# Performance work log

Hardware: AMD Instinct MI355X
Metric: run time of the kernel (lower is better)

## Reference

```python
import jax, jax.numpy as jnp
import numpy as np

NODE_TYPES = ["drug", "protein", "side_effect", "pathway"]
N = {"drug": 20000, "protein": 50000, "side_effect": 10000, "pathway": 3000}
# (src_type, dst_type) for: treats, targets, in_pathway, causes, rev_treats, rev_targets, rev_in_pathway
RELS = [("drug", "side_effect"), ("drug", "protein"), ("protein", "pathway"),
        ("protein", "side_effect"), ("side_effect", "drug"), ("protein", "drug"),
        ("pathway", "protein")]
E = [500000, 400000, 150000, 400000, 500000, 400000, 150000]
D_IN, H, O = 128, 256, 256
EPS = 1e-5


def setup_inputs() -> dict:
    key = jax.random.key(0)
    ks = iter(jax.random.split(key, 64))
    inp = {}
    for t in NODE_TYPES:
        inp["x_" + t] = jax.random.normal(next(ks), (N[t], D_IN), jnp.float32)
    for i, (st, dt) in enumerate(RELS):
        inp[f"src_{i}"] = jax.random.randint(next(ks), (E[i],), 0, N[st], jnp.int32)
        inp[f"dst_{i}"] = jax.random.randint(next(ks), (E[i],), 0, N[dt], jnp.int32)
    sc1 = float(1.0 / np.sqrt(D_IN))
    sc2 = float(1.0 / np.sqrt(H))
    inp["W1l"] = jax.random.uniform(next(ks), (7, D_IN, H), jnp.float32, -sc1, sc1)
    inp["W1r"] = jax.random.uniform(next(ks), (7, D_IN, H), jnp.float32, -sc1, sc1)
    inp["b1"] = jax.random.uniform(next(ks), (7, H), jnp.float32, -sc1, sc1)
    inp["W2l"] = jax.random.uniform(next(ks), (7, H, O), jnp.float32, -sc2, sc2)
    inp["W2r"] = jax.random.uniform(next(ks), (7, H, O), jnp.float32, -sc2, sc2)
    inp["b2"] = jax.random.uniform(next(ks), (7, O), jnp.float32, -sc2, sc2)
    inp["g1"] = jnp.ones((H,), jnp.float32)
    inp["beta1"] = jnp.zeros((H,), jnp.float32)
    inp["g2"] = jnp.ones((O,), jnp.float32)
    inp["beta2"] = jnp.zeros((O,), jnp.float32)
    return inp


def _sage_layer(xs, srcs, dsts, Wl, Wr, b):
    # Hetero SAGEConv: per relation, mean-aggregate src features at dst,
    # project, add root transform; sum over relations per dst type.
    out = {t: None for t in NODE_TYPES}
    for i, (st, dt) in enumerate(RELS):
        msg = xs[st][srcs[i]]                                             # [E_i, d] gather
        s = jax.ops.segment_sum(msg, dsts[i], num_segments=N[dt])         # scatter-add
        cnt = jax.ops.segment_sum(jnp.ones((msg.shape[0], 1), msg.dtype),
                                  dsts[i], num_segments=N[dt])
        mean = s / jnp.maximum(cnt, 1.0)                                  # SAGE default aggr='mean'
        rel = mean @ Wl[i] + b[i] + xs[dt] @ Wr[i]                        # lin_l(agg) + lin_r(x_dst)
        out[dt] = rel if out[dt] is None else out[dt] + rel               # HeteroConv aggr='sum'
    return out


def _bn_relu(v, g, beta):
    # training-mode BatchNorm1d (biased variance) + ReLU
    mu = v.mean(0)
    var = v.var(0)
    return jax.nn.relu((v - mu) * jax.lax.rsqrt(var + EPS) * g + beta)


def reference(x_drug, x_protein, x_side_effect, x_pathway,
              W1l, W1r, b1, W2l, W2r, b2, g1, beta1, g2, beta2,
              src_0, dst_0, src_1, dst_1, src_2, dst_2, src_3, dst_3,
              src_4, dst_4, src_5, dst_5, src_6, dst_6):
    xs = {"drug": x_drug, "protein": x_protein,
          "side_effect": x_side_effect, "pathway": x_pathway}
    srcs = [src_0, src_1, src_2, src_3, src_4, src_5, src_6]
    dsts = [dst_0, dst_1, dst_2, dst_3, dst_4, dst_5, dst_6]
    h = _sage_layer(xs, srcs, dsts, W1l, W1r, b1)
    h = {t: _bn_relu(v, g1, beta1) for t, v in h.items()}
    h = _sage_layer(h, srcs, dsts, W2l, W2r, b2)
    h = {t: _bn_relu(v, g2, beta2) for t, v in h.items()}
    return (h["drug"], h["protein"], h["side_effect"], h["pathway"])
```

## Files before the change

### kernel.cpp

```cpp
#include <hip/hip_runtime.h>

#define EPS_BN 1e-5f

typedef short bf16x8 __attribute__((ext_vector_type(8)));
typedef float f32x4 __attribute__((ext_vector_type(4)));

__device__ __forceinline__ unsigned short f2b(float f)
{
    union { float f; unsigned int u; } c; c.f = f;
    unsigned int u = c.u + 0x7FFFu + ((c.u >> 16) & 1u);
    return (unsigned short)(u >> 16);
}
__device__ __forceinline__ float blo(unsigned int u)
{
    union { unsigned int u; float f; } c; c.u = u << 16; return c.f;
}
__device__ __forceinline__ float bhi(unsigned int u)
{
    union { unsigned int u; float f; } c; c.u = u & 0xFFFF0000u; return c.f;
}

__device__ __forceinline__ void async_ld16(const unsigned short* g, unsigned short* l)
{
    __builtin_amdgcn_global_load_lds(
        (const __attribute__((address_space(1))) unsigned int*)g,
        (__attribute__((address_space(3))) unsigned int*)l, 16, 0, 0);
}

__device__ __forceinline__ int relof_e(int e) {
    return (e>=500000)+(e>=900000)+(e>=1050000)+(e>=1450000)+(e>=1950000)+(e>=2350000);
}
__device__ __forceinline__ int relof_n(int i) {
    return (i>=10000)+(i>=60000)+(i>=63000)+(i>=73000)+(i>=93000)+(i>=113000);
}
__device__ __forceinline__ int eoff_of(int r) {
    return r<1?0 : r<2?500000 : r<3?900000 : r<4?1050000 : r<5?1450000 : r<6?1950000 : 2350000;
}
__device__ __forceinline__ int coff_of(int r) {
    return r<1?0 : r<2?10000 : r<3?60000 : r<4?63000 : r<5?73000 : r<6?93000 : 113000;
}
__device__ __forceinline__ int typ_of(int row) { return (row>=20000)+(row>=70000)+(row>=80000); }
__device__ __forceinline__ int nbound(int t)   { return t<1?20000 : t<2?70000 : t<3?80000 : 83000; }
__device__ __forceinline__ float invR_of(int t){ return t<1?5e-5f : t<2?2e-5f : t<3?1e-4f : (1.0f/3000.0f); }

struct Graph { const int* src[7]; const int* dst[7]; };

__device__ __forceinline__ void relptrs(const Graph& g, int r, const int*& sp, const int*& dp)
{
    sp = g.src[0]; dp = g.dst[0];
    if (r==1){sp=g.src[1];dp=g.dst[1];}
    if (r==2){sp=g.src[2];dp=g.dst[2];}
    if (r==3){sp=g.src[3];dp=g.dst[3];}
    if (r==4){sp=g.src[4];dp=g.dst[4];}
    if (r==5){sp=g.src[5];dp=g.dst[5];}
    if (r==6){sp=g.src[6];dp=g.dst[6];}
}

__global__ void count_all(Graph g, int* __restrict__ icnt)
{
    for (int e = blockIdx.x * blockDim.x + threadIdx.x; e < 2500000; e += gridDim.x * blockDim.x) {
        int r = relof_e(e);
        const int *sp, *dp; relptrs(g, r, sp, dp);
        int le = e - eoff_of(r);
        atomicAdd(&icnt[coff_of(r) + dp[le]], 1);
    }
}

__global__ __launch_bounds__(1024)
void scan1(const int* __restrict__ icnt, int* __restrict__ scanbuf, int* __restrict__ bsums)
{
    __shared__ int lds[1024];
    int tid = threadIdx.x;
    int gid = blockIdx.x * 1024 + tid;
    int v = (gid < 163000) ? icnt[gid] : 0;
    lds[tid] = v;
    __syncthreads();
    for (int d = 1; d < 1024; d <<= 1) {
        int t = (tid >= d) ? lds[tid - d] : 0;
        __syncthreads();
        lds[tid] += t;
        __syncthreads();
    }
    scanbuf[gid] = lds[tid];
    if (tid == 1023) bsums[blockIdx.x] = lds[1023];
}

__global__ __launch_bounds__(256)
void scan2(int* __restrict__ bsums)
{
    __shared__ int lds[256];
    int tid = threadIdx.x;
    int v = (tid < 160) ? bsums[tid] : 0;
    lds[tid] = v;
    __syncthreads();
    for (int d = 1; d < 256; d <<= 1) {
        int t = (tid >= d) ? lds[tid - d] : 0;
        __syncthreads();
        lds[tid] += t;
        __syncthreads();
    }
    bsums[tid] = tid ? lds[tid - 1] : 0;
}

__global__ __launch_bounds__(256)
void scan_fix(const int* __restrict__ icnt, const int* __restrict__ scanbuf,
              const int* __restrict__ bsums, int* __restrict__ rowptrG,
              int* __restrict__ cur, float* __restrict__ inv,
              unsigned char* __restrict__ sliceid)
{
    int idx = blockIdx.x * blockDim.x + threadIdx.x;
    if (idx > 163000) return;
    int G = bsums[idx >> 10] + ((idx & 1023) ? scanbuf[idx - 1] : 0);
    rowptrG[idx] = G;
    if (idx < 163000) {
        cur[idx] = G;
        inv[idx] = 1.0f / (float)max(icnt[idx], 1);
        int s = G / 312500;
        sliceid[idx] = (unsigned char)(s > 7 ? 7 : s);
    }
}

__global__ void fill_all(Graph g, const unsigned char* __restrict__ sliceid,
                         int* __restrict__ cur, int* __restrict__ csr)
{
    const int slice = blockIdx.x & 7;
    const int bper  = gridDim.x >> 3;
    const int bidx  = blockIdx.x >> 3;
    for (int e = bidx * blockDim.x + threadIdx.x; e < 2500000; e += bper * blockDim.x) {
        int r = relof_e(e);
        const int *sp, *dp; relptrs(g, r, sp, dp);
        int le = e - eoff_of(r);
        int gidx = coff_of(r) + dp[le];
        if (sliceid[gidx] == slice)
            csr[atomicAdd(&cur[gidx], 1)] = sp[le];
    }
}

__global__ void tob16_kernel(const float* __restrict__ in, unsigned short* __restrict__ out, int n4)
{
    for (int i = blockIdx.x * blockDim.x + threadIdx.x; i < n4; i += gridDim.x * blockDim.x) {
        float4 v = ((const float4*)in)[i];
        uint2 o;
        o.x = (unsigned int)f2b(v.x) | ((unsigned int)f2b(v.y) << 16);
        o.y = (unsigned int)f2b(v.z) | ((unsigned int)f2b(v.w) << 16);
        ((uint2*)out)[i] = o;
    }
}

struct GatherCfg {
    const unsigned short* X[7];
    const int* rowptrG;
    const int* csr;
    const float* inv;
    unsigned short* agg;
};

template <int D>
__global__ __launch_bounds__(256)
void gather_all(GatherCfg c)
{
    constexpr int LPE = D / 8;
    constexpr int EPW = 64 / LPE;
    int wid = (blockIdx.x * blockDim.x + threadIdx.x) >> 6;
    if (wid >= 163000) return;
    int l = threadIdx.x & 63;
    int q = l & (LPE - 1);
    int gg = l / LPE;
    int r = relof_n(wid);
    const unsigned short* X = c.X[0];
    if (r==1) X=c.X[1];
    if (r==2) X=c.X[2];
    if (r==3) X=c.X[3];
    if (r==4) X=c.X[4];
    if (r==5) X=c.X[5];
    if (r==6) X=c.X[6];
    const unsigned short* Xq = X + q * 8;
    const int* csr = c.csr;
    int beg = c.rowptrG[wid], end = c.rowptrG[wid + 1];
    float acc[8] = {0.f,0.f,0.f,0.f,0.f,0.f,0.f,0.f};
    int it = beg;
    for (; it + 4 * EPW <= end; it += 4 * EPW) {
        int s0 = csr[it + gg];
        int s1 = csr[it + EPW + gg];
        int s2 = csr[it + 2 * EPW + gg];
        int s3 = csr[it + 3 * EPW + gg];
        uint4 v0 = *(const uint4*)(Xq + (size_t)s0 * D);
        uint4 v1 = *(const uint4*)(Xq + (size_t)s1 * D);
        uint4 v2 = *(const uint4*)(Xq + (size_t)s2 * D);
        uint4 v3 = *(const uint4*)(Xq + (size_t)s3 * D);
        acc[0]+=blo(v0.x); acc[1]+=bhi(v0.x); acc[2]+=blo(v0.y); acc[3]+=bhi(v0.y);
        acc[4]+=blo(v0.z); acc[5]+=bhi(v0.z); acc[6]+=blo(v0.w); acc[7]+=bhi(v0.w);
        acc[0]+=blo(v1.x); acc[1]+=bhi(v1.x); acc[2]+=blo(v1.y); acc[3]+=bhi(v1.y);
        acc[4]+=blo(v1.z); acc[5]+=bhi(v1.z); acc[6]+=blo(v1.w); acc[7]+=bhi(v1.w);
        acc[0]+=blo(v2.x); acc[1]+=bhi(v2.x); acc[2]+=blo(v2.y); acc[3]+=bhi(v2.y);
        acc[4]+=blo(v2.z); acc[5]+=bhi(v2.z); acc[6]+=blo(v2.w); acc[7]+=bhi(v2.w);
        acc[0]+=blo(v3.x); acc[1]+=bhi(v3.x); acc[2]+=blo(v3.y); acc[3]+=bhi(v3.y);
        acc[4]+=blo(v3.z); acc[5]+=bhi(v3.z); acc[6]+=blo(v3.w); acc[7]+=bhi(v3.w);
    }
    for (; it < end; it += EPW) {
        int i0 = it + gg;
        if (i0 < end) {
            int s0 = csr[i0];
            uint4 v0 = *(const uint4*)(Xq + (size_t)s0 * D);
            acc[0]+=blo(v0.x); acc[1]+=bhi(v0.x); acc[2]+=blo(v0.y); acc[3]+=bhi(v0.y);
            acc[4]+=blo(v0.z); acc[5]+=bhi(v0.z); acc[6]+=blo(v0.w); acc[7]+=bhi(v0.w);
        }
    }
#pragma unroll
    for (int k = 0; k < 8; ++k) {
        if (LPE == 16) acc[k] += __shfl_xor(acc[k], 16);
        acc[k] += __shfl_xor(acc[k], 32);
    }
    if (l < LPE) {
        float inv = c.inv[wid];
        uint4 o;
        o.x = (unsigned int)f2b(acc[0]*inv) | ((unsigned int)f2b(acc[1]*inv) << 16);
        o.y = (unsigned int)f2b(acc[2]*inv) | ((unsigned int)f2b(acc[3]*inv) << 16);
        o.z = (unsigned int)f2b(acc[4]*inv) | ((unsigned int)f2b(acc[5]*inv) << 16);
        o.w = (unsigned int)f2b(acc[6]*inv) | ((unsigned int)f2b(acc[7]*inv) << 16);
        *(uint4*)(c.agg + (size_t)wid * D + q * 8) = o;
    }
}

__global__ void wtrans_kernel(const float* __restrict__ Wr, const float* __restrict__ Wl,
                              unsigned short* __restrict__ wsumT, unsigned short* __restrict__ WlT,
                              int K)
{
    const int nrel[4]  = {2, 2, 2, 1};
    const int rl[4][2] = {{4,5},{1,6},{0,3},{2,2}};
    int per = 256 * K;
    int tot = 11 * per;
    for (int idx = blockIdx.x * blockDim.x + threadIdx.x; idx < tot;
         idx += gridDim.x * blockDim.x) {
        if (idx < 4 * per) {
            int t = idx / per, rem = idx - t * per;
            int n = rem / K, k = rem - n * K;
            float s = Wr[(size_t)rl[t][0] * per + k * 256 + n];
            if (nrel[t] > 1) s += Wr[(size_t)rl[t][1] * per + k * 256 + n];
            wsumT[idx] = f2b(s);
        } else {
            int j = idx - 4 * per;
            int r = j / per, rem = j - r * per;
            int n = rem / K, k = rem - n * K;
            WlT[j] = f2b(Wl[(size_t)r * per + k * 256 + n]);
        }
    }
}

struct GemmBatch {
    const unsigned short* A0[4];
    const unsigned short* A1[4];
    const unsigned short* A2[4];
    const unsigned short* B0[4];
    const unsigned short* B1[4];
    const unsigned short* B2[4];
    float* outF;
    unsigned short* outB;
    int R[4]; int bcum[4]; int rowoff[4]; int nsrc[4];
    int K, kshift, outf32;
};

__global__ __launch_bounds__(512, 4)
void gemm_mfma(GemmBatch g)
{
    __shared__ __align__(16) unsigned short Atile[2][128 * 32];
    __shared__ __align__(16) unsigned short Btile[2][256 * 32];

    const int tid = threadIdx.x;
    const int bz = blockIdx.x;
    const int t = (bz >= g.bcum[1]) + (bz >= g.bcum[2]) + (bz >= g.bcum[3]);
    const int bm = (bz - g.bcum[t]) << 7;
    const int w = tid >> 6, l = tid & 63;
    const int wr = w >> 2, wc = w & 3;

    const int R = g.R[t];
    const int K = g.K, kshift = g.kshift, kmask = K - 1;
    const unsigned short* A0t = g.A0[t];
    const unsigned short* A1t = g.A1[t];
    const unsigned short* A2t = g.A2[t];
    const unsigned short* B0t = g.B0[t];
    const unsigned short* B1t = g.B1[t];
    const unsigned short* B2t = g.B2[t];
    const int steps = (g.nsrc[t] * K) >> 5;

    const int rloc = tid >> 2;
    const int swz  = (((tid & 3) ^ ((tid >> 3) & 3)) << 3);
    const int srowA = min(bm + rloc, R - 1);
    const int wseg  = w << 9;

    auto stage = [&](int st, int buf) {
        int kglob = st << 5;
        int s  = kglob >> kshift;
        int kk = kglob & kmask;
        const unsigned short* As = (s == 0) ? A0t : (s == 1) ? A1t : A2t;
        const unsigned short* Bs = (s == 0) ? B0t : (s == 1) ? B1t : B2t;
        async_ld16(As + (size_t)srowA * K + kk + swz, &Atile[buf][wseg]);
        async_ld16(Bs + (size_t)rloc  * K + kk + swz, &Btile[buf][wseg]);
        async_ld16(Bs + (size_t)(128 + rloc) * K + kk + swz, &Btile[buf][4096 + wseg]);
    };

    f32x4 acc[4][4];
#pragma unroll
    for (int i = 0; i < 4; ++i)
#pragma unroll
        for (int j = 0; j < 4; ++j)
            acc[i][j] = (f32x4){0.f, 0.f, 0.f, 0.f};

    const int ck = l >> 4;
    const int ra = wr * 64 + (l & 15);
    const int aoff = ra * 32 + ((ck ^ ((ra >> 1) & 3)) << 3);
    const int rb = wc * 64 + (l & 15);
    const int boff = rb * 32 + ((ck ^ ((rb >> 1) & 3)) << 3);

    stage(0, 0);
    __syncthreads();
    int cur = 0;
    for (int st = 0; st < steps; ++st) {
        if (st + 1 < steps) stage(st + 1, cur ^ 1);
        const unsigned short* At = Atile[cur];
        const unsigned short* Bt = Btile[cur];
        bf16x8 af[4], bfr[4];
#pragma unroll
        for (int i = 0; i < 4; ++i) {
            af[i]  = *(const bf16x8*)(At + aoff + i * 512);
            bfr[i] = *(const bf16x8*)(Bt + boff + i * 512);
        }
#pragma unroll
        for (int mi = 0; mi < 4; ++mi)
#pragma unroll
            for (int ni = 0; ni < 4; ++ni)
                acc[mi][ni] = __builtin_amdgcn_mfma_f32_16x16x32_bf16(
                    af[mi], bfr[ni], acc[mi][ni], 0, 0, 0);
        __syncthreads();
        cur ^= 1;
    }

    const int orow0 = bm + wr * 64 + ((l >> 4) << 2);
    const int ocol0 = wc * 64 + (l & 15);
#pragma unroll
    for (int ni = 0; ni < 4; ++ni) {
        int col = ocol0 + ni * 16;
#pragma unroll
        for (int mi = 0; mi < 4; ++mi) {
#pragma unroll
            for (int j = 0; j < 4; ++j) {
                int row = orow0 + mi * 16 + j;
                if (row < R) {
                    float v = acc[mi][ni][j];
                    size_t o = (size_t)(g.rowoff[t] + row) * 256 + col;
                    if (g.outf32) g.outF[o] = v;
                    else          g.outB[o] = f2b(v);
                }
            }
        }
    }
}

template <int F32>
__global__ __launch_bounds__(256)
void bn_stats_all(const void* __restrict__ Hv, float* __restrict__ stats)
{
    int c = threadIdx.x;
    int r0 = blockIdx.x * 128;
    int r1 = min(r0 + 128, 83000);
    int t = typ_of(r0);
    int nb = nbound(t);
    float s = 0.f, ss = 0.f;
    for (int r = r0; r < r1; ++r) {
        if (r == nb) {
            atomicAdd(&stats[t * 512 + c], s);
            atomicAdd(&stats[t * 512 + 256 + c], ss);
            s = ss = 0.f; ++t; nb = nbound(t);
        }
        float v;
        if (F32) v = ((const float*)Hv)[(size_t)r * 256 + c];
        else { unsigned int u = ((const unsigned short*)Hv)[(size_t)r * 256 + c]; v = blo(u); }
        s += v; ss += v * v;
    }
    atomicAdd(&stats[t * 512 + c], s);
    atomicAdd(&stats[t * 512 + 256 + c], ss);
}

template <int F32>
__global__ __launch_bounds__(256)
void bn_apply_all(void* __restrict__ Hv, const float* __restrict__ stats,
                  const float* __restrict__ gg, const float* __restrict__ be)
{
    const int total4 = 83000 * 64;
    for (int i4 = blockIdx.x * blockDim.x + threadIdx.x; i4 < total4;
         i4 += gridDim.x * blockDim.x) {
        int row = i4 >> 6;
        int c4  = (i4 & 63) << 2;
        int t   = typ_of(row);
        float invR = invR_of(t);
        const float* st = stats + t * 512;
        float vin[4];
        if (F32) {
            float4 v = *(const float4*)((const float*)Hv + (size_t)row * 256 + c4);
            vin[0]=v.x; vin[1]=v.y; vin[2]=v.z; vin[3]=v.w;
        } else {
            uint2 u = *(const uint2*)((const unsigned short*)Hv + (size_t)row * 256 + c4);
            vin[0]=blo(u.x); vin[1]=bhi(u.x); vin[2]=blo(u.y); vin[3]=bhi(u.y);
        }
        float vout[4];
#pragma unroll
        for (int k = 0; k < 4; ++k) {
            int c = c4 + k;
            float mu  = st[c] * invR;
            float var = st[256 + c] * invR - mu * mu;
            float sc  = rsqrtf(var + EPS_BN) * gg[c];
            float v   = (vin[k] - mu) * sc + be[c];
            vout[k] = fmaxf(v, 0.f);
        }
        if (F32) {
            float4 o; o.x=vout[0]; o.y=vout[1]; o.z=vout[2]; o.w=vout[3];
            *(float4*)((float*)Hv + (size_t)row * 256 + c4) = o;
        } else {
            uint2 o;
            o.x = (unsigned int)f2b(vout[0]) | ((unsigned int)f2b(vout[1]) << 16);
            o.y = (unsigned int)f2b(vout[2]) | ((unsigned int)f2b(vout[3]) << 16);
            *(uint2*)((unsigned short*)Hv + (size_t)row * 256 + c4) = o;
        }
    }
}

extern "C" void kernel_launch(void* const* d_in, const int* in_sizes, int n_in,
                              void* d_out, int out_size, void* d_ws, size_t ws_size,
                              hipStream_t stream)
{
    static const int Nn[4]   = {20000, 50000, 10000, 3000};
    static const int roff[4] = {0, 20000, 70000, 80000};
    static const int rst[7]  = {0, 0, 1, 1, 2, 1, 3};
    static const int coff[7] = {0, 10000, 60000, 63000, 73000, 93000, 113000};
    static const int trels[4][2] = {{4,5},{1,6},{0,3},{2,2}};
    static const int tnrel[4]    = {2, 2, 2, 1};
    const int CNT_TOTAL = 163000;

    const float* x[4];
    for (int t = 0; t < 4; ++t) x[t] = (const float*)d_in[t];
    Graph graph;
    for (int i = 0; i < 7; ++i) {
        graph.src[i] = (const int*)d_in[4 + 2 * i];
        graph.dst[i] = (const int*)d_in[5 + 2 * i];
    }
    const float* W1l = (const float*)d_in[18];
    const float* W1r = (const float*)d_in[19];
    const float* W2l = (const float*)d_in[21];
    const float* W2r = (const float*)d_in[22];
    const float* g1  = (const float*)d_in[24];
    const float* be1 = (const float*)d_in[25];
    const float* g2  = (const float*)d_in[26];
    const float* be2 = (const float*)d_in[27];
    float* out = (float*)d_out;
    (void)n_in; (void)in_sizes; (void)out_size; (void)ws_size;

    char* w = (char*)d_ws;
    size_t off = 0;
    auto carve = [&](size_t bytes) -> void* {
        void* p = (void*)(w + off);
        off = (off + bytes + 255) & ~(size_t)255;
        return p;
    };
    int*   icnt    = (int*)carve((size_t)CNT_TOTAL * 4);
    int*   cur     = (int*)carve((size_t)CNT_TOTAL * 4);
    int*   rowptrG = (int*)carve((size_t)(CNT_TOTAL + 1) * 4);
    int*   csr     = (int*)carve((size_t)2500000 * 4);
    int*   scanbuf = (int*)carve((size_t)163840 * 4);
    int*   bsums   = (int*)carve((size_t)256 * 4);
    float* inv     = (float*)carve((size_t)CNT_TOTAL * 4);
    float* stats   = (float*)carve((size_t)4 * 512 * 4);
    unsigned char* sliceid = (unsigned char*)carve((size_t)CNT_TOTAL);
    unsigned short* wsumT = (unsigned short*)carve((size_t)4 * 256 * 256 * 2);
    unsigned short* WlT   = (unsigned short*)carve((size_t)7 * 256 * 256 * 2);
    unsigned short* U     = (unsigned short*)carve((size_t)163000 * 256 * 2);
    unsigned short* hb    = (unsigned short*)carve((size_t)83000 * 256 * 2);
    unsigned short* xb    = U;
    unsigned short* aggL1 = U + (size_t)83000 * 128;
    unsigned short* aggL2 = U;

    hipMemsetAsync(icnt, 0, (size_t)CNT_TOTAL * 4, stream);
    count_all<<<2048, 256, 0, stream>>>(graph, icnt);
    scan1<<<160, 1024, 0, stream>>>(icnt, scanbuf, bsums);
    scan2<<<1, 256, 0, stream>>>(bsums);
    scan_fix<<<(CNT_TOTAL + 256) / 256, 256, 0, stream>>>(icnt, scanbuf, bsums,
                                                          rowptrG, cur, inv, sliceid);
    fill_all<<<2048, 256, 0, stream>>>(graph, sliceid, cur, csr);

    for (int t = 0; t < 4; ++t)
        tob16_kernel<<<512, 256, 0, stream>>>(x[t], xb + (size_t)roff[t] * 128, Nn[t] * 32);

    for (int layer = 0; layer < 2; ++layer) {
        const int K = layer ? 256 : 128;
        const float* Wl = layer ? W2l : W1l;
        const float* Wr = layer ? W2r : W1r;
        const float* gg = layer ? g2  : g1;
        const float* be = layer ? be2 : be1;
        unsigned short* agg = layer ? aggL2 : aggL1;

        wtrans_kernel<<<1024, 256, 0, stream>>>(Wr, Wl, wsumT, WlT, K);

        GatherCfg gc;
        for (int r = 0; r < 7; ++r)
            gc.X[r] = layer ? (hb + (size_t)roff[rst[r]] * 256)
                            : (xb + (size_t)roff[rst[r]] * 128);
        gc.rowptrG = rowptrG; gc.csr = csr; gc.inv = inv; gc.agg = agg;
        if (layer == 0) gather_all<128><<<40750, 256, 0, stream>>>(gc);
        else            gather_all<256><<<40750, 256, 0, stream>>>(gc);

        GemmBatch gb;
        for (int t = 0; t < 4; ++t) {
            gb.A0[t] = layer ? (hb + (size_t)roff[t] * 256) : (xb + (size_t)roff[t] * 128);
            gb.A1[t] = agg + (size_t)coff[trels[t][0]] * K;
            gb.A2[t] = (tnrel[t] > 1) ? (agg + (size_t)coff[trels[t][1]] * K) : gb.A1[t];
            gb.B0[t] = wsumT + (size_t)t * 256 * K;
            gb.B1[t] = WlT + (size_t)trels[t][0] * 256 * K;
            gb.B2[t] = (tnrel[t] > 1) ? (WlT + (size_t)trels[t][1] * 256 * K) : gb.B1[t];
            gb.R[t] = Nn[t];
            gb.rowoff[t] = roff[t];
            gb.nsrc[t] = 1 + tnrel[t];
        }
        gb.bcum[0] = 0; gb.bcum[1] = 157; gb.bcum[2] = 548; gb.bcum[3] = 627;
        gb.outF = out; gb.outB = hb;
        gb.K = K; gb.kshift = layer ? 8 : 7; gb.outf32 = layer;
        gemm_mfma<<<651, 512, 0, stream>>>(gb);

        hipMemsetAsync(stats, 0, (size_t)4 * 512 * 4, stream);
        if (layer == 0) {
            bn_stats_all<0><<<649, 256, 0, stream>>>(hb, stats);
            bn_apply_all<0><<<2048, 256, 0, stream>>>(hb, stats, gg, be);
        } else {
            bn_stats_all<1><<<649, 256, 0, stream>>>(out, stats);
            bn_apply_all<1><<<2048, 256, 0, stream>>>(out, stats, gg, be);
        }
    }
}
```

Measured before the change: 864.1 us.

## Fuse BN stats into GEMM epilogue, merge conversions, dot2 gather accumulate

```diff
diff --git a/kernel.cpp b/kernel.cpp
--- a/kernel.cpp
+++ b/kernel.cpp
@@ -20,6 +20,12 @@
     union { unsigned int u; float f; } c; c.u = u & 0xFFFF0000u; return c.f;
 }
 
+__device__ __forceinline__ float dot2bf(float acc, unsigned int a, unsigned int sel)
+{
+    asm("v_dot2_f32_bf16 %0, %1, %2, %0" : "+v"(acc) : "v"(a), "v"(sel));
+    return acc;
+}
+
 __device__ __forceinline__ void async_ld16(const unsigned short* g, unsigned short* l)
 {
     __builtin_amdgcn_global_load_lds(
@@ -40,7 +46,6 @@
     return r<1?0 : r<2?10000 : r<3?60000 : r<4?63000 : r<5?73000 : r<6?93000 : 113000;
 }
 __device__ __forceinline__ int typ_of(int row) { return (row>=20000)+(row>=70000)+(row>=80000); }
-__device__ __forceinline__ int nbound(int t)   { return t<1?20000 : t<2?70000 : t<3?80000 : 83000; }
 __device__ __forceinline__ float invR_of(int t){ return t<1?5e-5f : t<2?2e-5f : t<3?1e-4f : (1.0f/3000.0f); }
 
 struct Graph { const int* src[7]; const int* dst[7]; };
@@ -136,14 +141,21 @@
     }
 }
 
-__global__ void tob16_kernel(const float* __restrict__ in, unsigned short* __restrict__ out, int n4)
-{
-    for (int i = blockIdx.x * blockDim.x + threadIdx.x; i < n4; i += gridDim.x * blockDim.x) {
-        float4 v = ((const float4*)in)[i];
+__global__ void tob16_all(const float* __restrict__ x0, const float* __restrict__ x1,
+                          const float* __restrict__ x2, const float* __restrict__ x3,
+                          unsigned short* __restrict__ xb)
+{
+    const int total = 83000 * 32;
+    for (int i = blockIdx.x * blockDim.x + threadIdx.x; i < total; i += gridDim.x * blockDim.x) {
+        int row = i >> 5, c4 = i & 31;
+        int t = typ_of(row);
+        const float* xp = (t == 0) ? x0 : (t == 1) ? x1 : (t == 2) ? x2 : x3;
+        int lrow = row - (t < 1 ? 0 : t < 2 ? 20000 : t < 3 ? 70000 : 80000);
+        float4 v = ((const float4*)(xp + (size_t)lrow * 128))[c4];
         uint2 o;
         o.x = (unsigned int)f2b(v.x) | ((unsigned int)f2b(v.y) << 16);
         o.y = (unsigned int)f2b(v.z) | ((unsigned int)f2b(v.w) << 16);
-        ((uint2*)out)[i] = o;
+        ((uint2*)(xb + (size_t)row * 128))[c4] = o;
     }
 }
 
@@ -161,6 +173,7 @@
 {
     constexpr int LPE = D / 8;
     constexpr int EPW = 64 / LPE;
+    constexpr int U   = 4;
     int wid = (blockIdx.x * blockDim.x + threadIdx.x) >> 6;
     if (wid >= 163000) return;
     int l = threadIdx.x & 63;
@@ -178,32 +191,30 @@
     const int* csr = c.csr;
     int beg = c.rowptrG[wid], end = c.rowptrG[wid + 1];
     float acc[8] = {0.f,0.f,0.f,0.f,0.f,0.f,0.f,0.f};
-    int it = beg;
-    for (; it + 4 * EPW <= end; it += 4 * EPW) {
-        int s0 = csr[it + gg];
-        int s1 = csr[it + EPW + gg];
-        int s2 = csr[it + 2 * EPW + gg];
-        int s3 = csr[it + 3 * EPW + gg];
-        uint4 v0 = *(const uint4*)(Xq + (size_t)s0 * D);
-        uint4 v1 = *(const uint4*)(Xq + (size_t)s1 * D);
-        uint4 v2 = *(const uint4*)(Xq + (size_t)s2 * D);
-        uint4 v3 = *(const uint4*)(Xq + (size_t)s3 * D);
-        acc[0]+=blo(v0.x); acc[1]+=bhi(v0.x); acc[2]+=blo(v0.y); acc[3]+=bhi(v0.y);
-        acc[4]+=blo(v0.z); acc[5]+=bhi(v0.z); acc[6]+=blo(v0.w); acc[7]+=bhi(v0.w);
-        acc[0]+=blo(v1.x); acc[1]+=bhi(v1.x); acc[2]+=blo(v1.y); acc[3]+=bhi(v1.y);
-        acc[4]+=blo(v1.z); acc[5]+=bhi(v1.z); acc[6]+=blo(v1.w); acc[7]+=bhi(v1.w);
-        acc[0]+=blo(v2.x); acc[1]+=bhi(v2.x); acc[2]+=blo(v2.y); acc[3]+=bhi(v2.y);
-        acc[4]+=blo(v2.z); acc[5]+=bhi(v2.z); acc[6]+=blo(v2.w); acc[7]+=bhi(v2.w);
-        acc[0]+=blo(v3.x); acc[1]+=bhi(v3.x); acc[2]+=blo(v3.y); acc[3]+=bhi(v3.y);
-        acc[4]+=blo(v3.z); acc[5]+=bhi(v3.z); acc[6]+=blo(v3.w); acc[7]+=bhi(v3.w);
-    }
-    for (; it < end; it += EPW) {
-        int i0 = it + gg;
-        if (i0 < end) {
-            int s0 = csr[i0];
-            uint4 v0 = *(const uint4*)(Xq + (size_t)s0 * D);
-            acc[0]+=blo(v0.x); acc[1]+=bhi(v0.x); acc[2]+=blo(v0.y); acc[3]+=bhi(v0.y);
-            acc[4]+=blo(v0.z); acc[5]+=bhi(v0.z); acc[6]+=blo(v0.w); acc[7]+=bhi(v0.w);
+    if (beg < end) {
+        const int last = end - 1;
+        for (int it = beg; it < end; it += U * EPW) {
+            uint4 v[U]; unsigned int sl[U];
+#pragma unroll
+            for (int j = 0; j < U; ++j) {
+                int idx = it + j * EPW + gg;
+                int e = idx < last ? idx : last;
+                int s = csr[e];
+                v[j]  = *(const uint4*)(Xq + (size_t)s * D);
+                sl[j] = (idx <= last) ? 0x00003F80u : 0u;
+            }
+#pragma unroll
+            for (int j = 0; j < U; ++j) {
+                unsigned int lo = sl[j], hi = sl[j] << 16;
+                acc[0] = dot2bf(acc[0], v[j].x, lo);
+                acc[1] = dot2bf(acc[1], v[j].x, hi);
+                acc[2] = dot2bf(acc[2], v[j].y, lo);
+                acc[3] = dot2bf(acc[3], v[j].y, hi);
+                acc[4] = dot2bf(acc[4], v[j].z, lo);
+                acc[5] = dot2bf(acc[5], v[j].z, hi);
+                acc[6] = dot2bf(acc[6], v[j].w, lo);
+                acc[7] = dot2bf(acc[7], v[j].w, hi);
+            }
         }
     }
 #pragma unroll
@@ -256,6 +267,7 @@
     const unsigned short* B2[4];
     float* outF;
     unsigned short* outB;
+    float* stats;
     int R[4]; int bcum[4]; int rowoff[4]; int nsrc[4];
     int K, kshift, outf32;
 };
@@ -340,45 +352,28 @@
 #pragma unroll
     for (int ni = 0; ni < 4; ++ni) {
         int col = ocol0 + ni * 16;
+        float ps = 0.f, pq = 0.f;
 #pragma unroll
         for (int mi = 0; mi < 4; ++mi) {
 #pragma unroll
             for (int j = 0; j < 4; ++j) {
                 int row = orow0 + mi * 16 + j;
+                float v = acc[mi][ni][j];
                 if (row < R) {
-                    float v = acc[mi][ni][j];
                     size_t o = (size_t)(g.rowoff[t] + row) * 256 + col;
                     if (g.outf32) g.outF[o] = v;
                     else          g.outB[o] = f2b(v);
-                }
+                } else v = 0.f;
+                ps += v; pq += v * v;
             }
         }
-    }
-}
-
-template <int F32>
-__global__ __launch_bounds__(256)
-void bn_stats_all(const void* __restrict__ Hv, float* __restrict__ stats)
-{
-    int c = threadIdx.x;
-    int r0 = blockIdx.x * 128;
-    int r1 = min(r0 + 128, 83000);
-    int t = typ_of(r0);
-    int nb = nbound(t);
-    float s = 0.f, ss = 0.f;
-    for (int r = r0; r < r1; ++r) {
-        if (r == nb) {
-            atomicAdd(&stats[t * 512 + c], s);
-            atomicAdd(&stats[t * 512 + 256 + c], ss);
-            s = ss = 0.f; ++t; nb = nbound(t);
-        }
-        float v;
-        if (F32) v = ((const float*)Hv)[(size_t)r * 256 + c];
-        else { unsigned int u = ((const unsigned short*)Hv)[(size_t)r * 256 + c]; v = blo(u); }
-        s += v; ss += v * v;
-    }
-    atomicAdd(&stats[t * 512 + c], s);
-    atomicAdd(&stats[t * 512 + 256 + c], ss);
+        ps += __shfl_xor(ps, 16); ps += __shfl_xor(ps, 32);
+        pq += __shfl_xor(pq, 16); pq += __shfl_xor(pq, 32);
+        if (l < 16) {
+            atomicAdd(&g.stats[t * 512 + col], ps);
+            atomicAdd(&g.stats[t * 512 + 256 + col], pq);
+        }
+    }
 }
 
 template <int F32>
@@ -468,17 +463,22 @@
     int*   scanbuf = (int*)carve((size_t)163840 * 4);
     int*   bsums   = (int*)carve((size_t)256 * 4);
     float* inv     = (float*)carve((size_t)CNT_TOTAL * 4);
-    float* stats   = (float*)carve((size_t)4 * 512 * 4);
+    float* stats   = (float*)carve((size_t)2 * 4 * 512 * 4);
     unsigned char* sliceid = (unsigned char*)carve((size_t)CNT_TOTAL);
-    unsigned short* wsumT = (unsigned short*)carve((size_t)4 * 256 * 256 * 2);
-    unsigned short* WlT   = (unsigned short*)carve((size_t)7 * 256 * 256 * 2);
-    unsigned short* U     = (unsigned short*)carve((size_t)163000 * 256 * 2);
-    unsigned short* hb    = (unsigned short*)carve((size_t)83000 * 256 * 2);
+    unsigned short* wsumT1 = (unsigned short*)carve((size_t)4 * 256 * 128 * 2);
+    unsigned short* WlT1   = (unsigned short*)carve((size_t)7 * 256 * 128 * 2);
+    unsigned short* wsumT2 = (unsigned short*)carve((size_t)4 * 256 * 256 * 2);
+    unsigned short* WlT2   = (unsigned short*)carve((size_t)7 * 256 * 256 * 2);
+    unsigned short* U      = (unsigned short*)carve((size_t)163000 * 256 * 2);
+    unsigned short* hb     = (unsigned short*)carve((size_t)83000 * 256 * 2);
     unsigned short* xb    = U;
     unsigned short* aggL1 = U + (size_t)83000 * 128;
     unsigned short* aggL2 = U;
+    float* stats1 = stats;
+    float* stats2 = stats + 2048;
 
     hipMemsetAsync(icnt, 0, (size_t)CNT_TOTAL * 4, stream);
+    hipMemsetAsync(stats, 0, (size_t)2 * 4 * 512 * 4, stream);
     count_all<<<2048, 256, 0, stream>>>(graph, icnt);
     scan1<<<160, 1024, 0, stream>>>(icnt, scanbuf, bsums);
     scan2<<<1, 256, 0, stream>>>(bsums);
@@ -486,18 +486,18 @@
                                                           rowptrG, cur, inv, sliceid);
     fill_all<<<2048, 256, 0, stream>>>(graph, sliceid, cur, csr);
 
-    for (int t = 0; t < 4; ++t)
-        tob16_kernel<<<512, 256, 0, stream>>>(x[t], xb + (size_t)roff[t] * 128, Nn[t] * 32);
+    tob16_all<<<2048, 256, 0, stream>>>(x[0], x[1], x[2], x[3], xb);
+    wtrans_kernel<<<1024, 256, 0, stream>>>(W1r, W1l, wsumT1, WlT1, 128);
+    wtrans_kernel<<<1024, 256, 0, stream>>>(W2r, W2l, wsumT2, WlT2, 256);
 
     for (int layer = 0; layer < 2; ++layer) {
         const int K = layer ? 256 : 128;
-        const float* Wl = layer ? W2l : W1l;
-        const float* Wr = layer ? W2r : W1r;
         const float* gg = layer ? g2  : g1;
         const float* be = layer ? be2 : be1;
         unsigned short* agg = layer ? aggL2 : aggL1;
-
-        wtrans_kernel<<<1024, 256, 0, stream>>>(Wr, Wl, wsumT, WlT, K);
+        unsigned short* wsumT = layer ? wsumT2 : wsumT1;
+        unsigned short* WlT   = layer ? WlT2   : WlT1;
+        float* st = layer ? stats2 : stats1;
 
         GatherCfg gc;
         for (int r = 0; r < 7; ++r)
@@ -521,16 +521,11 @@
         }
         gb.bcum[0] = 0; gb.bcum[1] = 157; gb.bcum[2] = 548; gb.bcum[3] = 627;
         gb.outF = out; gb.outB = hb;
+        gb.stats = st;
         gb.K = K; gb.kshift = layer ? 8 : 7; gb.outf32 = layer;
         gemm_mfma<<<651, 512, 0, stream>>>(gb);
 
-        hipMemsetAsync(stats, 0, (size_t)4 * 512 * 4, stream);
-        if (layer == 0) {
-            bn_stats_all<0><<<649, 256, 0, stream>>>(hb, stats);
-            bn_apply_all<0><<<2048, 256, 0, stream>>>(hb, stats, gg, be);
-        } else {
-            bn_stats_all<1><<<649, 256, 0, stream>>>(out, stats);
-            bn_apply_all<1><<<2048, 256, 0, stream>>>(out, stats, gg, be);
-        }
-    }
-}
+        if (layer == 0) bn_apply_all<0><<<2048, 256, 0, stream>>>(hb, st, gg, be);
+        else            bn_apply_all<1><<<2048, 256, 0, stream>>>(out, st, gg, be);
+    }
+}
```

After: 778.6 us, median of 2. 9.9% less time.
